# Performance work log

Hardware: AMD Instinct MI355X
Metric: run time of the kernel (lower is better)

The kernel has to match this reference:

```python
import jax, jax.numpy as jnp
import numpy as np

Q_DIM, KV_DIM, N_HEAD, C, OUT_DIM, N_AXIS = 256, 256, 8, 32, 256, 1
B, S = 1, 2048

def setup_inputs() -> dict:
    key = jax.random.key(0)
    ks = jax.random.split(key, 9)
    sd = 0.05
    return {
        "q_inputs": jax.random.normal(ks[0], (B, S, Q_DIM), jnp.float32),
        "kv_inputs": jax.random.normal(ks[1], (B, S, KV_DIM), jnp.float32),
        "bias": jax.random.normal(ks[2], (B, N_HEAD, S, S), jnp.float32),
        "qg_weights": jax.random.normal(ks[3], (Q_DIM, N_AXIS, N_HEAD, 2 * C), jnp.float32) * sd,
        "kv_weights": jax.random.normal(ks[4], (KV_DIM, N_AXIS, N_HEAD, 2 * C), jnp.float32) * sd,
        "qg_bias": jax.random.normal(ks[5], (N_AXIS, N_HEAD, 1, 2 * C), jnp.float32) * sd,
        "kv_bias": jax.random.normal(ks[6], (N_AXIS, N_HEAD, 1, 2 * C), jnp.float32) * sd,
        "o_weights": jax.random.normal(ks[7], (N_AXIS, N_HEAD, C, OUT_DIM), jnp.float32) * sd,
        "o_bias": jax.random.normal(ks[8], (OUT_DIM, N_AXIS), jnp.float32) * sd,
    }

def reference(q_inputs, kv_inputs, bias, qg_weights, kv_weights, qg_bias, kv_bias, o_weights, o_bias):
    scale = C ** (-0.5)
    # to_unsqueeze path: add axis dim r (=n_axis=1)
    qi = q_inputs[..., None]          # (B, q, q_dim, r)
    ki = kv_inputs[..., None]         # (B, k, kv_dim, r)
    b = bias[:, None]                 # (B, 1, h, q, k) broadcasts over r
    # per-axis, per-head QKV projections with bias
    qg = jnp.einsum('bqar,arhc->brhqc', qi, qg_weights) + qg_bias
    q, g = jnp.split(qg, 2, axis=-1)  # (B, r, h, q, c) each
    kv = jnp.einsum('bkar,arhc->brhkc', ki, kv_weights) + kv_bias
    k, v = jnp.split(kv, 2, axis=-1)  # (B, r, h, k, c) each
    logits = jnp.einsum('brhqc,brhkc->brhqk', q * scale, k) + b
    attn = jax.nn.softmax(logits, axis=-1)
    attn_out = jnp.einsum('brhqk,brhkc->brhqc', attn, v)
    attn_out = attn_out * jax.nn.sigmoid(g)  # gating
    output = jnp.einsum('brhqc,rhco->bqor', attn_out, o_weights) + o_bias
    return output[..., 0]  # squeeze the n_axis dim (to_unsqueeze path)
```

## Files before the change

### kernel.cpp

```cpp
#include <hip/hip_runtime.h>
#include <hip/hip_bf16.h>
#include <math.h>

#define SEQ   2048
#define NHEAD 8

typedef __attribute__((ext_vector_type(8))) short bf16x8;
typedef __attribute__((ext_vector_type(4))) short bf16x4;
typedef __attribute__((ext_vector_type(4))) float f32x4;

static __device__ __forceinline__ short f2bf(float f) {
    __hip_bfloat16 h = __float2bfloat16(f);
    return *reinterpret_cast<short*>(&h);
}

__global__ __launch_bounds__(256)
void prep_kernel(const float* __restrict__ q_in, const float* __restrict__ kv_in,
                 const float* __restrict__ qg_w, const float* __restrict__ kv_w,
                 const float* __restrict__ o_w,
                 short* __restrict__ qA, short* __restrict__ kvA,
                 short* __restrict__ wqgT, short* __restrict__ wkvT,
                 short* __restrict__ owT)
{
    const int i = blockIdx.x * 256 + threadIdx.x;
    if (i < 524288) {
        qA[i] = f2bf(q_in[i]);
    } else if (i < 1048576) {
        const int j = i - 524288;
        kvA[j] = f2bf(kv_in[j]);
    } else if (i < 1179648) {
        const int j = i - 1048576, n = j >> 8, k = j & 255;
        wqgT[j] = f2bf(qg_w[k * 512 + n]);
    } else if (i < 1310720) {
        const int j = i - 1179648, n = j >> 8, k = j & 255;
        wkvT[j] = f2bf(kv_w[k * 512 + n]);
    } else if (i < 1376256) {
        const int j = i - 1310720, n = j >> 8, k = j & 255;
        owT[j] = f2bf(o_w[k * 256 + n]);
    }
}

__global__ __launch_bounds__(256)
void proj_qgkv_kernel(const short* __restrict__ qA, const short* __restrict__ kvA,
                      const short* __restrict__ wqgT, const short* __restrict__ wkvT,
                      const float* __restrict__ qg_b, const float* __restrict__ kv_b,
                      short* __restrict__ qs, float* __restrict__ gs,
                      short* __restrict__ ks, short* __restrict__ vT)
{
    const int z = blockIdx.z;
    const short* __restrict__ A  = z ? kvA  : qA;
    const short* __restrict__ W  = z ? wkvT : wqgT;
    const float* __restrict__ bv = z ? kv_b : qg_b;

    const int tid = threadIdx.x;
    const int wq = tid >> 6, lane = tid & 63;
    const int ln = lane & 15, quad = lane >> 4;
    const int m0 = blockIdx.x << 6;
    const int n0 = blockIdx.y << 5;

    f32x4 acc[2];
#pragma unroll
    for (int nt = 0; nt < 2; nt++) {
        const float b = bv[n0 + (nt << 4) + ln];
        acc[nt] = (f32x4){b, b, b, b};
    }

    const short* ap = A + (size_t)(m0 + (wq << 4) + ln) * 256 + (quad << 3);
    for (int k8 = 0; k8 < 8; k8++) {
        bf16x8 a = *(const bf16x8*)(ap + k8 * 32);
#pragma unroll
        for (int nt = 0; nt < 2; nt++) {
            bf16x8 b = *(const bf16x8*)(W + (size_t)(n0 + (nt << 4) + ln) * 256
                                          + k8 * 32 + (quad << 3));
            acc[nt] = __builtin_amdgcn_mfma_f32_16x16x32_bf16(a, b, acc[nt], 0, 0, 0);
        }
    }

    const float scale = 0.17677669529663689f;
#pragma unroll
    for (int nt = 0; nt < 2; nt++) {
        const int n = n0 + (nt << 4) + ln;
        const int h = n >> 6, c2 = n & 63;
#pragma unroll
        for (int r = 0; r < 4; r++) {
            const int m = m0 + (wq << 4) + (quad << 2) + r;
            const float v = acc[nt][r];
            if (z == 0) {
                if (c2 < 32) qs[(((h << 11) + m) << 5) + c2] = f2bf(v * scale);
                else gs[(((h << 11) + m) << 5) + (c2 - 32)] = 1.0f / (1.0f + __expf(-v));
            } else {
                if (c2 < 32) ks[(((h << 11) + m) << 5) + c2] = f2bf(v);
                else vT[(((h << 5) + (c2 - 32)) << 11) + m] = f2bf(v);
            }
        }
    }
}

__global__ __launch_bounds__(256)
void attn_kernel(const short* __restrict__ qs, const short* __restrict__ ks,
                 const short* __restrict__ vT, const float* __restrict__ bias,
                 float* __restrict__ Opart, float* __restrict__ mpart,
                 float* __restrict__ lpart, int ksize)
{
    const int h = blockIdx.y, z = blockIdx.z;
    const int q0 = blockIdx.x << 6;
    const int tid = threadIdx.x;
    const int wq = tid >> 6, lane = tid & 63;
    const int ln = lane & 15, quad = lane >> 4;

    __shared__ float blds[4][16][68];

    const int qrow = q0 + (wq << 4) + ln;
    const bf16x8 qf = *(const bf16x8*)(qs + (((size_t)(h << 11) + qrow) << 5) + (quad << 3));

    const float L2E = 1.44269504088896f;
    float ml2 = -1e30f, l = 0.f;
    f32x4 O0 = {0, 0, 0, 0}, O1 = {0, 0, 0, 0};

    const int kbeg = z * ksize;
    const int ntile = ksize >> 6;
    const size_t bias_row0 = ((size_t)h * SEQ + q0 + (wq << 4)) * SEQ;

    for (int kt = 0; kt < ntile; kt++) {
        const int k0 = kbeg + (kt << 6);

#pragma unroll
        for (int p = 0; p < 4; p++) {
            const int row = (quad << 2) + p;
            float4 b4 = *(const float4*)(bias + bias_row0 + (size_t)row * SEQ
                                         + k0 + (ln << 2));
            *(float4*)&blds[wq][row][ln << 2] = b4;
        }
        bf16x8 kf[4];
#pragma unroll
        for (int mt = 0; mt < 4; mt++)
            kf[mt] = *(const bf16x8*)(ks + (((size_t)(h << 11) + k0 + (mt << 4) + ln) << 5)
                                         + (quad << 3));
        bf16x4 vh[2][2][2];
#pragma unroll
        for (int cm = 0; cm < 2; cm++) {
            const size_t vb = (((size_t)(h << 5) + (cm << 4) + ln) << 11) + k0 + (quad << 2);
#pragma unroll
            for (int kc = 0; kc < 2; kc++)
#pragma unroll
                for (int hf = 0; hf < 2; hf++)
                    vh[cm][kc][hf] = *(const bf16x4*)(vT + vb + (kc << 5) + (hf << 4));
        }

        f32x4 S[4];
#pragma unroll
        for (int mt = 0; mt < 4; mt++) {
            f32x4 c = *(const f32x4*)&blds[wq][ln][(mt << 4) + (quad << 2)];
            S[mt] = __builtin_amdgcn_mfma_f32_16x16x32_bf16(kf[mt], qf, c, 0, 0, 0);
        }

        float smax = S[0][0];
#pragma unroll
        for (int mt = 0; mt < 4; mt++)
#pragma unroll
            for (int r = 0; r < 4; r++) smax = fmaxf(smax, S[mt][r]);
        smax = fmaxf(smax, __shfl_xor(smax, 16));
        smax = fmaxf(smax, __shfl_xor(smax, 32));
        const float mnew = fmaxf(ml2, smax * L2E);
        const float alpha = exp2f(ml2 - mnew);
        ml2 = mnew;

        float pr[4][4];
        float rs = 0.f;
#pragma unroll
        for (int mt = 0; mt < 4; mt++)
#pragma unroll
            for (int r = 0; r < 4; r++) {
                const float p = exp2f(fmaf(S[mt][r], L2E, -mnew));
                pr[mt][r] = p;
                rs += p;
            }
        rs += __shfl_xor(rs, 16);
        rs += __shfl_xor(rs, 32);
        l = l * alpha + rs;

        short pb[4][4];
#pragma unroll
        for (int mt = 0; mt < 4; mt++)
#pragma unroll
            for (int r = 0; r < 4; r++) pb[mt][r] = f2bf(pr[mt][r]);
        bf16x8 P0 = {pb[0][0], pb[0][1], pb[0][2], pb[0][3],
                     pb[1][0], pb[1][1], pb[1][2], pb[1][3]};
        bf16x8 P1 = {pb[2][0], pb[2][1], pb[2][2], pb[2][3],
                     pb[3][0], pb[3][1], pb[3][2], pb[3][3]};

        O0 *= alpha;
        O1 *= alpha;
#pragma unroll
        for (int kc = 0; kc < 2; kc++) {
            const bf16x8 P = kc ? P1 : P0;
            bf16x8 va0 = __builtin_shufflevector(vh[0][kc][0], vh[0][kc][1],
                                                 0, 1, 2, 3, 4, 5, 6, 7);
            bf16x8 va1 = __builtin_shufflevector(vh[1][kc][0], vh[1][kc][1],
                                                 0, 1, 2, 3, 4, 5, 6, 7);
            O0 = __builtin_amdgcn_mfma_f32_16x16x32_bf16(va0, P, O0, 0, 0, 0);
            O1 = __builtin_amdgcn_mfma_f32_16x16x32_bf16(va1, P, O1, 0, 0, 0);
        }
    }

    const size_t pb_ = (((size_t)(z * NHEAD + h)) << 11) + qrow;
    if (quad == 0) { mpart[pb_] = ml2; lpart[pb_] = l; }
    float* op = Opart + (pb_ << 5);
#pragma unroll
    for (int r = 0; r < 4; r++) {
        op[(quad << 2) + r]      = O0[r];
        op[16 + (quad << 2) + r] = O1[r];
    }
}

__global__ __launch_bounds__(256)
void combine_kernel(const float* __restrict__ Opart, const float* __restrict__ mpart,
                    const float* __restrict__ lpart, const float* __restrict__ gs,
                    short* __restrict__ att, int nsplit)
{
    const int g  = blockIdx.x * 256 + threadIdx.x;
    const int c4 = g & 7;
    const int q  = (g >> 3) & (SEQ - 1);
    const int h  = g >> 14;

    float M = -1e30f;
    for (int s = 0; s < nsplit; s++)
        M = fmaxf(M, mpart[(((size_t)s * NHEAD + h) << 11) + q]);

    float l = 0.f;
    float4 O = {0.f, 0.f, 0.f, 0.f};
    for (int s = 0; s < nsplit; s++) {
        const size_t base = (((size_t)s * NHEAD + h) << 11) + q;
        const float w = exp2f(mpart[base] - M);
        l += w * lpart[base];
        float4 o4 = *(const float4*)(Opart + (base << 5) + (c4 << 2));
        O.x = fmaf(w, o4.x, O.x); O.y = fmaf(w, o4.y, O.y);
        O.z = fmaf(w, o4.z, O.z); O.w = fmaf(w, o4.w, O.w);
    }
    const float inv = 1.0f / l;
    float4 g4 = *(const float4*)(gs + ((((size_t)h << 11) + q) << 5) + (c4 << 2));
    bf16x4 r;
    r[0] = f2bf(O.x * inv * g4.x); r[1] = f2bf(O.y * inv * g4.y);
    r[2] = f2bf(O.z * inv * g4.z); r[3] = f2bf(O.w * inv * g4.w);
    *(bf16x4*)(att + ((size_t)q << 8) + (h << 5) + (c4 << 2)) = r;
}

__global__ __launch_bounds__(256)
void proj_o_kernel(const short* __restrict__ att, const short* __restrict__ owT,
                   const float* __restrict__ o_b, float* __restrict__ out)
{
    const int tid = threadIdx.x;
    const int wq = tid >> 6, lane = tid & 63;
    const int ln = lane & 15, quad = lane >> 4;
    const int m0 = blockIdx.x << 6;
    const int n0 = blockIdx.y << 4;

    const int n = n0 + ln;
    const float b = o_b[n];
    f32x4 acc = (f32x4){b, b, b, b};

    const short* ap = att + (size_t)(m0 + (wq << 4) + ln) * 256 + (quad << 3);
    const short* bp = owT + (size_t)n * 256 + (quad << 3);
    for (int k8 = 0; k8 < 8; k8++) {
        bf16x8 a = *(const bf16x8*)(ap + k8 * 32);
        bf16x8 w = *(const bf16x8*)(bp + k8 * 32);
        acc = __builtin_amdgcn_mfma_f32_16x16x32_bf16(a, w, acc, 0, 0, 0);
    }
#pragma unroll
    for (int r = 0; r < 4; r++) {
        const int m = m0 + (wq << 4) + (quad << 2) + r;
        out[(size_t)m * 256 + n] = acc[r];
    }
}

extern "C" void kernel_launch(void* const* d_in, const int* in_sizes, int n_in,
                              void* d_out, int out_size, void* d_ws, size_t ws_size,
                              hipStream_t stream)
{
    const float* q_in  = (const float*)d_in[0];
    const float* kv_in = (const float*)d_in[1];
    const float* bias  = (const float*)d_in[2];
    const float* qg_w  = (const float*)d_in[3];
    const float* kv_w  = (const float*)d_in[4];
    const float* qg_b  = (const float*)d_in[5];
    const float* kv_b  = (const float*)d_in[6];
    const float* o_w   = (const float*)d_in[7];
    const float* o_b   = (const float*)d_in[8];
    float* out = (float*)d_out;

    char* p = (char*)d_ws;
    short* qs   = (short*)p; p += 1048576;
    short* ksb  = (short*)p; p += 1048576;
    short* vTb  = (short*)p; p += 1048576;
    short* attb = (short*)p; p += 1048576;
    short* qA   = (short*)p; p += 1048576;
    short* kvA  = (short*)p; p += 1048576;
    short* wqgT = (short*)p; p += 262144;
    short* wkvT = (short*)p; p += 262144;
    short* owT  = (short*)p; p += 131072;
    float* gs   = (float*)p; p += 2097152;

    const size_t fixed = (size_t)(p - (char*)d_ws);
    int nsplit = 1;
    {
        const int cand[3] = {4, 2, 1};
        for (int i = 0; i < 3; i++) {
            size_t ns = (size_t)cand[i];
            if (fixed + ns * (2097152 + 131072) <= ws_size) { nsplit = cand[i]; break; }
        }
    }
    float* mp = (float*)p;
    float* lp = mp + (size_t)nsplit * NHEAD * SEQ;
    float* Op = lp + (size_t)nsplit * NHEAD * SEQ;

    hipLaunchKernelGGL(prep_kernel, dim3(5376), dim3(256), 0, stream,
                       q_in, kv_in, qg_w, kv_w, o_w, qA, kvA, wqgT, wkvT, owT);
    hipLaunchKernelGGL(proj_qgkv_kernel, dim3(32, 16, 2), dim3(256), 0, stream,
                       qA, kvA, wqgT, wkvT, qg_b, kv_b, qs, gs, ksb, vTb);
    hipLaunchKernelGGL(attn_kernel, dim3(32, NHEAD, nsplit), dim3(256), 0, stream,
                       qs, ksb, vTb, bias, Op, mp, lp, SEQ / nsplit);
    hipLaunchKernelGGL(combine_kernel, dim3(512), dim3(256), 0, stream,
                       Op, mp, lp, gs, attb, nsplit);
    hipLaunchKernelGGL(proj_o_kernel, dim3(32, 16), dim3(256), 0, stream,
                       attb, owT, o_b, out);
}
```

Baseline: 248.1 us.

## Fuse input bf16 conversion into projection, drop bias LDS staging, raise split-K

Replaces the monolithic prep kernel with a tiled LDS transpose that only converts the weights. The q/kv activation fp32-to-bf16 conversion now happens inside the projection kernel's loads, removing a full pass over the inputs and two workspace buffers. The attention kernel loads bias directly into the MFMA accumulator layout instead of staging it through shared memory, and adds an occupancy hint of 6 blocks per CU. The split-K candidate list gains 8, which adds parallelism at the cost of more combine work and partial-buffer traffic.

```diff
diff --git a/kernel.cpp b/kernel.cpp
--- a/kernel.cpp
+++ b/kernel.cpp
@@ -15,40 +15,40 @@
 }
 
 __global__ __launch_bounds__(256)
-void prep_kernel(const float* __restrict__ q_in, const float* __restrict__ kv_in,
-                 const float* __restrict__ qg_w, const float* __restrict__ kv_w,
-                 const float* __restrict__ o_w,
-                 short* __restrict__ qA, short* __restrict__ kvA,
-                 short* __restrict__ wqgT, short* __restrict__ wkvT,
-                 short* __restrict__ owT)
-{
-    const int i = blockIdx.x * 256 + threadIdx.x;
-    if (i < 524288) {
-        qA[i] = f2bf(q_in[i]);
-    } else if (i < 1048576) {
-        const int j = i - 524288;
-        kvA[j] = f2bf(kv_in[j]);
-    } else if (i < 1179648) {
-        const int j = i - 1048576, n = j >> 8, k = j & 255;
-        wqgT[j] = f2bf(qg_w[k * 512 + n]);
-    } else if (i < 1310720) {
-        const int j = i - 1179648, n = j >> 8, k = j & 255;
-        wkvT[j] = f2bf(kv_w[k * 512 + n]);
-    } else if (i < 1376256) {
-        const int j = i - 1310720, n = j >> 8, k = j & 255;
-        owT[j] = f2bf(o_w[k * 256 + n]);
-    }
+void prep_w_kernel(const float* __restrict__ qg_w, const float* __restrict__ kv_w,
+                   const float* __restrict__ o_w, short* __restrict__ wqgT,
+                   short* __restrict__ wkvT, short* __restrict__ owT)
+{
+    __shared__ float t[64][65];
+    int bid = blockIdx.x;
+    const float* src; short* dst; int N, tr, tc;
+    if (bid < 32)      { src = qg_w; dst = wqgT; N = 512; tr = bid >> 3; tc = bid & 7; }
+    else if (bid < 64) { bid -= 32; src = kv_w; dst = wkvT; N = 512; tr = bid >> 3; tc = bid & 7; }
+    else               { bid -= 64; src = o_w;  dst = owT;  N = 256; tr = bid >> 2; tc = bid & 3; }
+
+    const int tid = threadIdx.x;
+    const int rr = tid >> 6;
+    const int cc = tid & 63;
+#pragma unroll
+    for (int s = 0; s < 16; s++)
+        t[(s << 2) + rr][cc] =
+            src[(size_t)((tr << 6) + (s << 2) + rr) * N + (tc << 6) + cc];
+    __syncthreads();
+#pragma unroll
+    for (int s = 0; s < 16; s++)
+        dst[(size_t)((tc << 6) + (s << 2) + rr) * 256 + (tr << 6) + cc]
+            = f2bf(t[cc][(s << 2) + rr]);
 }
 
 __global__ __launch_bounds__(256)
-void proj_qgkv_kernel(const short* __restrict__ qA, const short* __restrict__ kvA,
+void proj_qgkv_kernel(const float* __restrict__ q_in, const float* __restrict__ kv_in,
                       const short* __restrict__ wqgT, const short* __restrict__ wkvT,
                       const float* __restrict__ qg_b, const float* __restrict__ kv_b,
                       short* __restrict__ qs, float* __restrict__ gs,
                       short* __restrict__ ks, short* __restrict__ vT)
 {
     const int z = blockIdx.z;
-    const short* __restrict__ A  = z ? kvA  : qA;
+    const float* __restrict__ A  = z ? kv_in : q_in;
     const short* __restrict__ W  = z ? wkvT : wqgT;
     const float* __restrict__ bv = z ? kv_b : qg_b;
 
@@ -65,13 +65,17 @@
         acc[nt] = (f32x4){b, b, b, b};
     }
 
-    const short* ap = A + (size_t)(m0 + (wq << 4) + ln) * 256 + (quad << 3);
+    const float* ap = A + (size_t)(m0 + (wq << 4) + ln) * 256 + (quad << 3);
     for (int k8 = 0; k8 < 8; k8++) {
-        bf16x8 a = *(const bf16x8*)(ap + k8 * 32);
+        float4 a0 = *(const float4*)(ap + (k8 << 5));
+        float4 a1 = *(const float4*)(ap + (k8 << 5) + 4);
+        bf16x8 a;
+        a[0] = f2bf(a0.x); a[1] = f2bf(a0.y); a[2] = f2bf(a0.z); a[3] = f2bf(a0.w);
+        a[4] = f2bf(a1.x); a[5] = f2bf(a1.y); a[6] = f2bf(a1.z); a[7] = f2bf(a1.w);
 #pragma unroll
         for (int nt = 0; nt < 2; nt++) {
             bf16x8 b = *(const bf16x8*)(W + (size_t)(n0 + (nt << 4) + ln) * 256
-                                          + k8 * 32 + (quad << 3));
+                                          + (k8 << 5) + (quad << 3));
             acc[nt] = __builtin_amdgcn_mfma_f32_16x16x32_bf16(a, b, acc[nt], 0, 0, 0);
         }
     }
@@ -96,7 +100,7 @@
     }
 }
 
-__global__ __launch_bounds__(256)
+__global__ __launch_bounds__(256, 6)
 void attn_kernel(const short* __restrict__ qs, const short* __restrict__ ks,
                  const short* __restrict__ vT, const float* __restrict__ bias,
                  float* __restrict__ Opart, float* __restrict__ mpart,
@@ -108,8 +112,6 @@
     const int wq = tid >> 6, lane = tid & 63;
     const int ln = lane & 15, quad = lane >> 4;
 
-    __shared__ float blds[4][16][68];
-
     const int qrow = q0 + (wq << 4) + ln;
     const bf16x8 qf = *(const bf16x8*)(qs + (((size_t)(h << 11) + qrow) << 5) + (quad << 3));
 
@@ -117,25 +119,22 @@
     float ml2 = -1e30f, l = 0.f;
     f32x4 O0 = {0, 0, 0, 0}, O1 = {0, 0, 0, 0};
 
-    const int kbeg = z * ksize;
+    const int kbeg  = z * ksize;
     const int ntile = ksize >> 6;
-    const size_t bias_row0 = ((size_t)h * SEQ + q0 + (wq << 4)) * SEQ;
+    const float* bp = bias + ((size_t)h * SEQ + qrow) * SEQ + kbeg + (quad << 2);
+    const short* kp = ks + (((size_t)(h << 11) + kbeg + ln) << 5) + (quad << 3);
 
     for (int kt = 0; kt < ntile; kt++) {
         const int k0 = kbeg + (kt << 6);
 
-#pragma unroll
-        for (int p = 0; p < 4; p++) {
-            const int row = (quad << 2) + p;
-            float4 b4 = *(const float4*)(bias + bias_row0 + (size_t)row * SEQ
-                                         + k0 + (ln << 2));
-            *(float4*)&blds[wq][row][ln << 2] = b4;
-        }
+        f32x4 cb[4];
+#pragma unroll
+        for (int mt = 0; mt < 4; mt++)
+            cb[mt] = *(const f32x4*)(bp + (kt << 6) + (mt << 4));
         bf16x8 kf[4];
 #pragma unroll
         for (int mt = 0; mt < 4; mt++)
-            kf[mt] = *(const bf16x8*)(ks + (((size_t)(h << 11) + k0 + (mt << 4) + ln) << 5)
-                                         + (quad << 3));
+            kf[mt] = *(const bf16x8*)(kp + (size_t)(((kt << 6) + (mt << 4)) << 5));
         bf16x4 vh[2][2][2];
 #pragma unroll
         for (int cm = 0; cm < 2; cm++) {
@@ -149,10 +148,8 @@
 
         f32x4 S[4];
 #pragma unroll
-        for (int mt = 0; mt < 4; mt++) {
-            f32x4 c = *(const f32x4*)&blds[wq][ln][(mt << 4) + (quad << 2)];
-            S[mt] = __builtin_amdgcn_mfma_f32_16x16x32_bf16(kf[mt], qf, c, 0, 0, 0);
-        }
+        for (int mt = 0; mt < 4; mt++)
+            S[mt] = __builtin_amdgcn_mfma_f32_16x16x32_bf16(kf[mt], qf, cb[mt], 0, 0, 0);
 
         float smax = S[0][0];
 #pragma unroll
@@ -261,9 +258,10 @@
 
     const short* ap = att + (size_t)(m0 + (wq << 4) + ln) * 256 + (quad << 3);
     const short* bp = owT + (size_t)n * 256 + (quad << 3);
+#pragma unroll
     for (int k8 = 0; k8 < 8; k8++) {
-        bf16x8 a = *(const bf16x8*)(ap + k8 * 32);
-        bf16x8 w = *(const bf16x8*)(bp + k8 * 32);
+        bf16x8 a = *(const bf16x8*)(ap + (k8 << 5));
+        bf16x8 w = *(const bf16x8*)(bp + (k8 << 5));
         acc = __builtin_amdgcn_mfma_f32_16x16x32_bf16(a, w, acc, 0, 0, 0);
     }
 #pragma unroll
@@ -293,8 +291,6 @@
     short* ksb  = (short*)p; p += 1048576;
     short* vTb  = (short*)p; p += 1048576;
     short* attb = (short*)p; p += 1048576;
-    short* qA   = (short*)p; p += 1048576;
-    short* kvA  = (short*)p; p += 1048576;
     short* wqgT = (short*)p; p += 262144;
     short* wkvT = (short*)p; p += 262144;
     short* owT  = (short*)p; p += 131072;
@@ -303,20 +299,22 @@
     const size_t fixed = (size_t)(p - (char*)d_ws);
     int nsplit = 1;
     {
-        const int cand[3] = {4, 2, 1};
-        for (int i = 0; i < 3; i++) {
+        const int cand[4] = {8, 4, 2, 1};
+        for (int i = 0; i < 4; i++) {
             size_t ns = (size_t)cand[i];
-            if (fixed + ns * (2097152 + 131072) <= ws_size) { nsplit = cand[i]; break; }
+            if (fixed + ns * (size_t)(2097152 + 2 * 65536) <= ws_size) {
+                nsplit = cand[i]; break;
+            }
         }
     }
     float* mp = (float*)p;
     float* lp = mp + (size_t)nsplit * NHEAD * SEQ;
     float* Op = lp + (size_t)nsplit * NHEAD * SEQ;
 
-    hipLaunchKernelGGL(prep_kernel, dim3(5376), dim3(256), 0, stream,
-                       q_in, kv_in, qg_w, kv_w, o_w, qA, kvA, wqgT, wkvT, owT);
+    hipLaunchKernelGGL(prep_w_kernel, dim3(80), dim3(256), 0, stream,
+                       qg_w, kv_w, o_w, wqgT, wkvT, owT);
     hipLaunchKernelGGL(proj_qgkv_kernel, dim3(32, 16, 2), dim3(256), 0, stream,
-                       qA, kvA, wqgT, wkvT, qg_b, kv_b, qs, gs, ksb, vTb);
+                       q_in, kv_in, wqgT, wkvT, qg_b, kv_b, qs, gs, ksb, vTb);
     hipLaunchKernelGGL(attn_kernel, dim3(32, NHEAD, nsplit), dim3(256), 0, stream,
                        qs, ksb, vTb, bias, Op, mp, lp, SEQ / nsplit);
     hipLaunchKernelGGL(combine_kernel, dim3(512), dim3(256), 0, stream,
```

After: 263.5 us. +6.2%, slower.
